# Kernel tuning notes

Hardware: AMD Instinct MI355X
Metric: run time of the kernel (lower is better)

## Reference

```python
import jax, jax.numpy as jnp
import numpy as np

B, K, D = 16384, 8, 64
NUM_USER, NUM_ENT, NUM_REL = 100000, 1000000, 32


def setup_inputs() -> dict:
    key = jax.random.key(0)
    ks = jax.random.split(key, 12)
    return {
        'u': jax.random.randint(ks[0], (B,), 0, NUM_USER, dtype=jnp.int32),
        'v': jax.random.randint(ks[1], (B,), 0, NUM_ENT, dtype=jnp.int32),
        'user_and_item_adj': jax.random.randint(ks[2], (B, K), 0, NUM_ENT, dtype=jnp.int32),
        'adj_ent': jax.random.randint(ks[3], (NUM_ENT, K), 0, NUM_ENT, dtype=jnp.int32),
        'adj_rel': jax.random.randint(ks[4], (NUM_ENT, K), 0, NUM_REL, dtype=jnp.int32),
        'usr_emb': jax.random.normal(ks[5], (NUM_USER, D), dtype=jnp.float32) * 0.02,
        'ent_emb': jax.random.normal(ks[6], (NUM_ENT, D), dtype=jnp.float32) * 0.02,
        'rel_emb': jax.random.normal(ks[7], (NUM_REL, D), dtype=jnp.float32) * 0.02,
        'conv_w': jax.random.normal(ks[8], (1, K, 3, 3), dtype=jnp.float32) * 0.1,  # OIHW
        'conv_b': jnp.zeros((1,), dtype=jnp.float32),
        'agg_w': jax.random.normal(ks[9], (D, D), dtype=jnp.float32) * 0.05,
        'agg_b': jnp.zeros((D,), dtype=jnp.float32),
    }


def reference(u, v, user_and_item_adj, adj_ent, adj_rel,
              usr_emb, ent_emb, rel_emb, conv_w, conv_b, agg_w, agg_b):
    # --- user-side: user emb * user-item-history entity embs, then conv2d ---
    uai = ent_emb[user_and_item_adj]                      # [B, K, D]
    ue = usr_emb[u][:, None, :] * uai                     # [B, K, D]
    x = ue[..., None]                                     # [B, K, D, 1]  (NCHW)
    y = jax.lax.conv_general_dilated(
        x, conv_w, window_strides=(1, 1), padding=((1, 1), (1, 1)),
        dimension_numbers=('NCHW', 'OIHW', 'NCHW'))      # [B, 1, D, 1]
    user_embeddings = y[:, 0, :, 0] + conv_b[0]           # [B, D]

    # --- item-side: one-hop neighbor gather + KGCN sum aggregator ---
    ent_idx = adj_ent[v]                                  # [B, K]
    rel_idx = adj_rel[v]                                  # [B, K]
    self_vec = ent_emb[v]                                 # [B, D]
    neigh = ent_emb[ent_idx]                              # [B, K, D]
    rels = rel_emb[rel_idx]                               # [B, K, D]

    # user-relation attention scores, softmax over K neighbors
    scores = jnp.einsum('bd,bkd->bk', user_embeddings, rels)   # [B, K]
    attn = jax.nn.softmax(scores, axis=-1)                     # [B, K]
    neigh_agg = jnp.einsum('bk,bkd->bd', attn, neigh)          # [B, D]

    # 'sum' aggregator: (self + neighbors) -> Linear -> sigmoid
    item_embeddings = jax.nn.sigmoid((self_vec + neigh_agg) @ agg_w + agg_b)  # [B, D]

    out = jax.nn.sigmoid(jnp.sum(user_embeddings * item_embeddings, axis=1))  # [B]
    return out
```

## Files before the change

### kernel.cpp

```cpp
#include <hip/hip_runtime.h>
#include <math.h>

__global__ __launch_bounds__(256) void pifsa_gnn_kernel(
    const int*   __restrict__ u,
    const int*   __restrict__ v,
    const int*   __restrict__ uai,
    const int*   __restrict__ adj_ent,
    const int*   __restrict__ adj_rel,
    const float* __restrict__ usr_emb,
    const float* __restrict__ ent_emb,
    const float* __restrict__ rel_emb,
    const float* __restrict__ conv_w,
    const float* __restrict__ conv_b,
    const float* __restrict__ agg_w,
    const float* __restrict__ agg_b,
    float*       __restrict__ out,
    int B)
{
    __shared__ float s_aggw[64 * 64];
    __shared__ float s_h[4][64];

    const int tid  = threadIdx.x;
    const int lane = tid & 63;
    const int wave = tid >> 6;

    for (int i = tid; i < 64 * 64; i += 256) s_aggw[i] = agg_w[i];
    __syncthreads();

    const int b      = blockIdx.x * 4 + wave;
    const bool live  = (b < B);
    const int bb     = live ? b : (B - 1);

    const int   ub  = u[bb];
    const float usr = usr_emb[ub * 64 + lane];

    float ue[8];
#pragma unroll
    for (int c = 0; c < 8; ++c) {
        const int e = uai[bb * 8 + c];
        ue[c] = usr * ent_emb[e * 64 + lane];
    }

    float user_e = conv_b[0];
#pragma unroll
    for (int c = 0; c < 8; ++c) {
        const float w0 = conv_w[c * 9 + 1];
        const float w1 = conv_w[c * 9 + 4];
        const float w2 = conv_w[c * 9 + 7];
        float prev = __shfl_up(ue[c], 1, 64);
        float next = __shfl_down(ue[c], 1, 64);
        if (lane == 0)  prev = 0.0f;
        if (lane == 63) next = 0.0f;
        user_e = fmaf(w0, prev, user_e);
        user_e = fmaf(w1, ue[c], user_e);
        user_e = fmaf(w2, next, user_e);
    }

    const int vb = v[bb];

    float sc[8];
#pragma unroll
    for (int k = 0; k < 8; ++k) {
        const int r = adj_rel[vb * 8 + k];
        float p = user_e * rel_emb[r * 64 + lane];
#pragma unroll
        for (int off = 32; off >= 1; off >>= 1)
            p += __shfl_xor(p, off, 64);
        sc[k] = p;
    }

    float m = sc[0];
#pragma unroll
    for (int k = 1; k < 8; ++k) m = fmaxf(m, sc[k]);
    float ek[8];
    float denom = 0.0f;
#pragma unroll
    for (int k = 0; k < 8; ++k) { ek[k] = __expf(sc[k] - m); denom += ek[k]; }
    const float inv_denom = 1.0f / denom;

    float h = ent_emb[vb * 64 + lane];
#pragma unroll
    for (int k = 0; k < 8; ++k) {
        const int n = adj_ent[vb * 8 + k];
        h = fmaf(ek[k] * inv_denom, ent_emb[n * 64 + lane], h);
    }

    s_h[wave][lane] = h;
    __syncthreads();

    float acc = agg_b[lane];
#pragma unroll 16
    for (int d = 0; d < 64; ++d)
        acc = fmaf(s_h[wave][d], s_aggw[d * 64 + lane], acc);
    const float item = 1.0f / (1.0f + __expf(-acc));

    float p = user_e * item;
#pragma unroll
    for (int off = 32; off >= 1; off >>= 1)
        p += __shfl_xor(p, off, 64);

    if (live && lane == 0)
        out[b] = 1.0f / (1.0f + __expf(-p));
}

extern "C" void kernel_launch(void* const* d_in, const int* in_sizes, int n_in,
                              void* d_out, int out_size, void* d_ws, size_t ws_size,
                              hipStream_t stream) {
    const int*   u        = (const int*)  d_in[0];
    const int*   v        = (const int*)  d_in[1];
    const int*   uai      = (const int*)  d_in[2];
    const int*   adj_ent  = (const int*)  d_in[3];
    const int*   adj_rel  = (const int*)  d_in[4];
    const float* usr_emb  = (const float*)d_in[5];
    const float* ent_emb  = (const float*)d_in[6];
    const float* rel_emb  = (const float*)d_in[7];
    const float* conv_w   = (const float*)d_in[8];
    const float* conv_b   = (const float*)d_in[9];
    const float* agg_w    = (const float*)d_in[10];
    const float* agg_b    = (const float*)d_in[11];
    float*       out      = (float*)d_out;

    const int B = in_sizes[0];
    const int grid = (B + 3) / 4;
    pifsa_gnn_kernel<<<grid, 256, 0, stream>>>(
        u, v, uai, adj_ent, adj_rel, usr_emb, ent_emb, rel_emb,
        conv_w, conv_b, agg_w, agg_b, out, B);
}
```

Baseline: 362.0 us.

## Vectorize per-row work with float4 lane groups and drop shared agg_w staging

Each wavefront still handles one batch row, but lanes are now split into four 16-lane groups. Each lane holds a float4 slice of the 64-wide embedding, and each group covers two of the eight neighbor channels. Gathers become 16-byte vector loads, and the conv, attention scores and aggregation are reduced across groups with a few cross-lane shuffles. The per-block copy of the 16KB agg_w matrix into shared memory and both __syncthreads calls are removed. The matvec instead reads agg_w directly from global memory, relying on cache, with h broadcast by shuffles. The trade-off is extra shuffle traffic and uncached-risk global reads of agg_w in exchange for much less redundant staging traffic and fewer load instructions.

```diff
diff --git a/kernel.cpp b/kernel.cpp
--- a/kernel.cpp
+++ b/kernel.cpp
@@ -1,5 +1,35 @@
 #include <hip/hip_runtime.h>
 #include <math.h>
+
+
+__device__ __forceinline__ float4 ld4(const float* p) {
+    return *reinterpret_cast<const float4*>(p);
+}
+__device__ __forceinline__ float dot4(float4 a, float4 b) {
+    return fmaf(a.x, b.x, fmaf(a.y, b.y, fmaf(a.z, b.z, a.w * b.w)));
+}
+__device__ __forceinline__ float4 fma4(float s, float4 a, float4 acc) {
+    acc.x = fmaf(s, a.x, acc.x);
+    acc.y = fmaf(s, a.y, acc.y);
+    acc.z = fmaf(s, a.z, acc.z);
+    acc.w = fmaf(s, a.w, acc.w);
+    return acc;
+}
+__device__ __forceinline__ float4 xgroup_sum4(float4 v) {
+    v.x += __shfl_xor(v.x, 16, 64); v.x += __shfl_xor(v.x, 32, 64);
+    v.y += __shfl_xor(v.y, 16, 64); v.y += __shfl_xor(v.y, 32, 64);
+    v.z += __shfl_xor(v.z, 16, 64); v.z += __shfl_xor(v.z, 32, 64);
+    v.w += __shfl_xor(v.w, 16, 64); v.w += __shfl_xor(v.w, 32, 64);
+    return v;
+}
+__device__ __forceinline__ float4 shfl4(float4 v, int src) {
+    float4 r;
+    r.x = __shfl(v.x, src, 64);
+    r.y = __shfl(v.y, src, 64);
+    r.z = __shfl(v.z, src, 64);
+    r.w = __shfl(v.w, src, 64);
+    return r;
+}
 
 __global__ __launch_bounds__(256) void pifsa_gnn_kernel(
     const int*   __restrict__ u,
@@ -17,90 +47,117 @@
     float*       __restrict__ out,
     int B)
 {
-    __shared__ float s_aggw[64 * 64];
-    __shared__ float s_h[4][64];
+    const int gtid = blockIdx.x * 256 + threadIdx.x;
+    const int b    = gtid >> 6;
+    if (b >= B) return;
 
-    const int tid  = threadIdx.x;
-    const int lane = tid & 63;
-    const int wave = tid >> 6;
+    const int l  = threadIdx.x & 63;
+    const int g  = l >> 4;
+    const int q  = l & 15;
+    const int d0 = q << 2;
 
-    for (int i = tid; i < 64 * 64; i += 256) s_aggw[i] = agg_w[i];
-    __syncthreads();
+    const int ub = u[b];
+    const int vb = v[b];
+    const int c0 = g, c1 = g + 4;
+    const int e0 = uai[b * 8 + c0];
+    const int e1 = uai[b * 8 + c1];
+    const int r0 = adj_rel[vb * 8 + c0];
+    const int r1 = adj_rel[vb * 8 + c1];
+    const int n0 = adj_ent[vb * 8 + c0];
+    const int n1 = adj_ent[vb * 8 + c1];
 
-    const int b      = blockIdx.x * 4 + wave;
-    const bool live  = (b < B);
-    const int bb     = live ? b : (B - 1);
+    const float4 usr = ld4(usr_emb + ub * 64 + d0);
+    float4 a0 = ld4(ent_emb + (size_t)e0 * 64 + d0);
+    float4 a1 = ld4(ent_emb + (size_t)e1 * 64 + d0);
+    float4 ue0, ue1;
+    ue0.x = usr.x * a0.x; ue0.y = usr.y * a0.y; ue0.z = usr.z * a0.z; ue0.w = usr.w * a0.w;
+    ue1.x = usr.x * a1.x; ue1.y = usr.y * a1.y; ue1.z = usr.z * a1.z; ue1.w = usr.w * a1.w;
 
-    const int   ub  = u[bb];
-    const float usr = usr_emb[ub * 64 + lane];
+    const float w0a = conv_w[c0 * 9 + 1], w1a = conv_w[c0 * 9 + 4], w2a = conv_w[c0 * 9 + 7];
+    const float w0b = conv_w[c1 * 9 + 1], w1b = conv_w[c1 * 9 + 4], w2b = conv_w[c1 * 9 + 7];
 
-    float ue[8];
+    float4 cacc = make_float4(0.f, 0.f, 0.f, 0.f);
+    {
+        float pw = __shfl(ue0.w, (l - 1) & 63, 64); if (q == 0)  pw = 0.f;
+        float nx = __shfl(ue0.x, (l + 1) & 63, 64); if (q == 15) nx = 0.f;
+        float4 prev = make_float4(pw, ue0.x, ue0.y, ue0.z);
+        float4 next = make_float4(ue0.y, ue0.z, ue0.w, nx);
+        cacc = fma4(w1a, ue0, cacc);
+        cacc = fma4(w0a, prev, cacc);
+        cacc = fma4(w2a, next, cacc);
+    }
+    {
+        float pw = __shfl(ue1.w, (l - 1) & 63, 64); if (q == 0)  pw = 0.f;
+        float nx = __shfl(ue1.x, (l + 1) & 63, 64); if (q == 15) nx = 0.f;
+        float4 prev = make_float4(pw, ue1.x, ue1.y, ue1.z);
+        float4 next = make_float4(ue1.y, ue1.z, ue1.w, nx);
+        cacc = fma4(w1b, ue1, cacc);
+        cacc = fma4(w0b, prev, cacc);
+        cacc = fma4(w2b, next, cacc);
+    }
+    cacc = xgroup_sum4(cacc);
+    const float cb = conv_b[0];
+    float4 user_e = make_float4(cacc.x + cb, cacc.y + cb, cacc.z + cb, cacc.w + cb);
+
+    float p0 = dot4(user_e, ld4(rel_emb + r0 * 64 + d0));
+    float p1 = dot4(user_e, ld4(rel_emb + r1 * 64 + d0));
 #pragma unroll
-    for (int c = 0; c < 8; ++c) {
-        const int e = uai[bb * 8 + c];
-        ue[c] = usr * ent_emb[e * 64 + lane];
+    for (int off = 1; off <= 8; off <<= 1) {
+        p0 += __shfl_xor(p0, off, 64);
+        p1 += __shfl_xor(p1, off, 64);
+    }
+    float s[8];
+#pragma unroll
+    for (int kk = 0; kk < 4; ++kk) {
+        s[kk]     = __shfl(p0, kk * 16, 64);
+        s[kk + 4] = __shfl(p1, kk * 16, 64);
     }
 
-    float user_e = conv_b[0];
+    float m = s[0];
 #pragma unroll
-    for (int c = 0; c < 8; ++c) {
-        const float w0 = conv_w[c * 9 + 1];
-        const float w1 = conv_w[c * 9 + 4];
-        const float w2 = conv_w[c * 9 + 7];
-        float prev = __shfl_up(ue[c], 1, 64);
-        float next = __shfl_down(ue[c], 1, 64);
-        if (lane == 0)  prev = 0.0f;
-        if (lane == 63) next = 0.0f;
-        user_e = fmaf(w0, prev, user_e);
-        user_e = fmaf(w1, ue[c], user_e);
-        user_e = fmaf(w2, next, user_e);
+    for (int k = 1; k < 8; ++k) m = fmaxf(m, s[k]);
+    float den = 0.f;
+    float ek[8];
+#pragma unroll
+    for (int k = 0; k < 8; ++k) { ek[k] = __expf(s[k] - m); den += ek[k]; }
+    const float inv_den = 1.f / den;
+    const float at0 = ek[c0] * inv_den;
+    const float at1 = ek[c1] * inv_den;
+
+    float4 nb0 = ld4(ent_emb + (size_t)n0 * 64 + d0);
+    float4 nb1 = ld4(ent_emb + (size_t)n1 * 64 + d0);
+    float4 hp = make_float4(0.f, 0.f, 0.f, 0.f);
+    hp = fma4(at0, nb0, hp);
+    hp = fma4(at1, nb1, hp);
+    hp = xgroup_sum4(hp);
+    const float4 self4 = ld4(ent_emb + (size_t)vb * 64 + d0);
+    float4 h4 = make_float4(self4.x + hp.x, self4.y + hp.y, self4.z + hp.z, self4.w + hp.w);
+
+    float4 acc = make_float4(0.f, 0.f, 0.f, 0.f);
+#pragma unroll
+    for (int i = 0; i < 4; ++i) {
+        const float4 hb = shfl4(h4, 20 * g + i);
+        const float* wrow = agg_w + (16 * g + 4 * i) * 64 + d0;
+        acc = fma4(hb.x, ld4(wrow),       acc);
+        acc = fma4(hb.y, ld4(wrow + 64),  acc);
+        acc = fma4(hb.z, ld4(wrow + 128), acc);
+        acc = fma4(hb.w, ld4(wrow + 192), acc);
     }
+    acc = xgroup_sum4(acc);
+    const float4 bias = ld4(agg_b + d0);
+    float4 item;
+    item.x = 1.f / (1.f + __expf(-(acc.x + bias.x)));
+    item.y = 1.f / (1.f + __expf(-(acc.y + bias.y)));
+    item.z = 1.f / (1.f + __expf(-(acc.z + bias.z)));
+    item.w = 1.f / (1.f + __expf(-(acc.w + bias.w)));
 
-    const int vb = v[bb];
-
-    float sc[8];
+    float p = dot4(user_e, item);
 #pragma unroll
-    for (int k = 0; k < 8; ++k) {
-        const int r = adj_rel[vb * 8 + k];
-        float p = user_e * rel_emb[r * 64 + lane];
-#pragma unroll
-        for (int off = 32; off >= 1; off >>= 1)
-            p += __shfl_xor(p, off, 64);
-        sc[k] = p;
-    }
-
-    float m = sc[0];
-#pragma unroll
-    for (int k = 1; k < 8; ++k) m = fmaxf(m, sc[k]);
-    float ek[8];
-    float denom = 0.0f;
-#pragma unroll
-    for (int k = 0; k < 8; ++k) { ek[k] = __expf(sc[k] - m); denom += ek[k]; }
-    const float inv_denom = 1.0f / denom;
-
-    float h = ent_emb[vb * 64 + lane];
-#pragma unroll
-    for (int k = 0; k < 8; ++k) {
-        const int n = adj_ent[vb * 8 + k];
-        h = fmaf(ek[k] * inv_denom, ent_emb[n * 64 + lane], h);
-    }
-
-    s_h[wave][lane] = h;
-    __syncthreads();
-
-    float acc = agg_b[lane];
-#pragma unroll 16
-    for (int d = 0; d < 64; ++d)
-        acc = fmaf(s_h[wave][d], s_aggw[d * 64 + lane], acc);
-    const float item = 1.0f / (1.0f + __expf(-acc));
-
-    float p = user_e * item;
-#pragma unroll
-    for (int off = 32; off >= 1; off >>= 1)
+    for (int off = 1; off <= 8; off <<= 1)
         p += __shfl_xor(p, off, 64);
 
-    if (live && lane == 0)
-        out[b] = 1.0f / (1.0f + __expf(-p));
+    if (l == 0)
+        out[b] = 1.f / (1.f + __expf(-p));
 }
 
 extern "C" void kernel_launch(void* const* d_in, const int* in_sizes, int n_in,
```

After: 357.7 us. About the same (-1.2%).
